# Optimization experiments

Hardware: AMD Instinct MI355X
Metric: run time of the kernel (lower is better)

Reference implementation:

```python
import jax, jax.numpy as jnp
import numpy as np

N, IN_DIM, HID, OUT = 100000, 256, 256, 128
E = 500000


def setup_inputs() -> dict:
    key = jax.random.key(0)
    ks = jax.random.split(key, 12)
    s_in = 1.0 / np.sqrt(IN_DIM)
    s_h = 1.0 / np.sqrt(HID)
    s_c = 1.0 / np.sqrt(2 * OUT)
    return {
        "x": jax.random.normal(ks[0], (N, IN_DIM), dtype=jnp.float32),
        "pos_u": jax.random.randint(ks[1], (E,), 0, N),
        "pos_v": jax.random.randint(ks[2], (E,), 0, N),
        "neg_u": jax.random.randint(ks[3], (E,), 0, N),
        "neg_v": jax.random.randint(ks[4], (E,), 0, N),
        "Wn1": jax.random.normal(ks[5], (IN_DIM, HID), dtype=jnp.float32) * s_in,
        "bn1": jnp.zeros((HID,), dtype=jnp.float32),
        "Wn2": jax.random.normal(ks[6], (HID, OUT), dtype=jnp.float32) * s_h,
        "bn2": jnp.zeros((OUT,), dtype=jnp.float32),
        "Ws1": jax.random.normal(ks[7], (2 * OUT, HID), dtype=jnp.float32) * s_c,
        "bs1": jnp.zeros((HID,), dtype=jnp.float32),
        "Ws2": jax.random.normal(ks[8], (HID, 1), dtype=jnp.float32) * s_h,
        "bs2": jnp.zeros((1,), dtype=jnp.float32),
    }


def _pair_logits(H, u, v, Ws1, bs1, Ws2, bs2):
    hu = H[u]  # [E, OUT] gather
    hv = H[v]
    feats = jnp.concatenate([jnp.abs(hu - hv), hu * hv], axis=-1)  # [E, 2*OUT]
    h = jax.nn.relu(feats @ Ws1 + bs1)
    return (h @ Ws2 + bs2)[..., 0]  # [E]


def reference(x, pos_u, pos_v, neg_u, neg_v,
              Wn1, bn1, Wn2, bn2, Ws1, bs1, Ws2, bs2):
    # node encoder MLP (dropout = identity in eval)
    H = jax.nn.relu(x @ Wn1 + bn1) @ Wn2 + bn2  # [N, OUT]
    pos_logit = _pair_logits(H, pos_u, pos_v, Ws1, bs1, Ws2, bs2)
    neg_logit = _pair_logits(H, neg_u, neg_v, Ws1, bs1, Ws2, bs2)
    return (pos_logit, neg_logit, H)
```

## Files before the change

### kernel.cpp

```cpp
#include <hip/hip_runtime.h>

typedef unsigned short u16;
typedef __bf16 bf16x8 __attribute__((ext_vector_type(8)));
typedef float f32x4 __attribute__((ext_vector_type(4)));
typedef unsigned int u32x4 __attribute__((ext_vector_type(4)));

#define MFMA16(a, b, c) __builtin_amdgcn_mfma_f32_16x16x32_bf16((a), (b), (c), 0, 0, 0)

#define NNODE 100000
#define EDGES 500000
#define NPAIR 1000000

__device__ __forceinline__ u16 bf16bits(float f) {
  __bf16 h = (__bf16)f;
  return __builtin_bit_cast(unsigned short, h);
}

__global__ void prep_weights(const float* __restrict__ Wn1,
                             const float* __restrict__ Wn2,
                             const float* __restrict__ Ws1,
                             u16* __restrict__ ws) {
  int gid = blockIdx.x * 256 + threadIdx.x;
  const float* src;
  int ldn;
  u16* dst;
  int e;
  if (gid < 65536) {
    src = Wn1; ldn = 256; dst = ws; e = gid;
  } else if (gid < 98304) {
    src = Wn2; ldn = 128; dst = ws + 65536; e = gid - 65536;
  } else {
    src = Ws1; ldn = 256; dst = ws + 98304; e = gid - 98304;
  }
  int j = e & 7;
  int lane = (e >> 3) & 63;
  int s = (e >> 9) & 7;
  int nt = e >> 12;
  int n = (nt << 4) | (lane & 15);
  int k = (s << 5) | (((lane >> 4) & 3) << 3) | j;
  dst[e] = bf16bits(src[k * ldn + n]);
}

__launch_bounds__(256, 2)
__global__ void node_kernel(const float* __restrict__ x,
                            const u16* __restrict__ WnT1,
                            const u16* __restrict__ WnT2,
                            const float* __restrict__ bn1,
                            const float* __restrict__ bn2,
                            float* __restrict__ Hout,
                            u16* __restrict__ Hb) {
  __shared__ __align__(16) u16 buf[32768];
  const int tid = threadIdx.x;
  const int w = tid >> 6, l = tid & 63;
  const int lg = l >> 4, ll = l & 15;
  const int rowbase = blockIdx.x * 128 + w * 32;

  bf16x8 af[2][8];
#pragma unroll
  for (int m = 0; m < 2; m++) {
    int r = rowbase + m * 16 + ll;
    if (r > NNODE - 1) r = NNODE - 1;
    const float* xp = x + (long)r * 256 + lg * 8;
#pragma unroll
    for (int c = 0; c < 8; c++) {
      f32x4 a0 = *(const f32x4*)(xp + c * 32);
      f32x4 a1 = *(const f32x4*)(xp + c * 32 + 4);
      bf16x8 d;
#pragma unroll
      for (int j = 0; j < 4; j++) {
        d[j] = (__bf16)a0[j];
        d[j + 4] = (__bf16)a1[j];
      }
      af[m][c] = d;
    }
  }

  f32x4 acc[2][16];
#pragma unroll
  for (int nh = 0; nh < 2; nh++) {
    if (nh) __syncthreads();
    {
      const u32x4* src = (const u32x4*)(WnT1 + nh * 32768);
      u32x4* dstv = (u32x4*)buf;
#pragma unroll
      for (int i = 0; i < 16; i++) dstv[tid + i * 256] = src[tid + i * 256];
    }
    __syncthreads();
#pragma unroll
    for (int nt = 0; nt < 8; nt++) {
      int n = nh * 128 + nt * 16 + ll;
      float bv = bn1[n];
      f32x4 a0 = {bv, bv, bv, bv}, a1 = a0;
      const u16* bp = buf + nt * 4096 + l * 8;
#pragma unroll
      for (int s = 0; s < 8; s++) {
        bf16x8 bw = *(const bf16x8*)(bp + s * 512);
        a0 = MFMA16(af[0][s], bw, a0);
        a1 = MFMA16(af[1][s], bw, a1);
      }
      acc[0][nh * 8 + nt] = a0;
      acc[1][nh * 8 + nt] = a1;
    }
  }
  __syncthreads();

  const int hbase = w * 8192;
#pragma unroll
  for (int m = 0; m < 2; m++) {
#pragma unroll
    for (int q = 0; q < 16; q++) {
      int s2 = q >> 1;
      int k3 = ((q & 1) << 1) | (ll >> 3);
      int j = ll & 7;
      f32x4 a = acc[m][q];
#pragma unroll
      for (int t = 0; t < 4; t++) {
        int lane2 = k3 * 16 + lg * 4 + t;
        buf[hbase + ((m * 8 + s2) * 64 + lane2) * 8 + j] = bf16bits(fmaxf(a[t], 0.f));
      }
    }
  }

#pragma unroll
  for (int m = 0; m < 2; m++) {
#pragma unroll
    for (int s = 0; s < 8; s++) {
      af[m][s] = *(const bf16x8*)(buf + hbase + ((m * 8 + s) * 64 + l) * 8);
    }
  }

#pragma unroll
  for (int nt = 0; nt < 8; nt++) {
    int n = nt * 16 + ll;
    float bv = bn2[n];
    f32x4 a0 = {bv, bv, bv, bv}, a1 = a0;
    const u16* bp = WnT2 + nt * 4096 + l * 8;
#pragma unroll
    for (int s = 0; s < 8; s++) {
      bf16x8 bw = *(const bf16x8*)(bp + s * 512);
      a0 = MFMA16(af[0][s], bw, a0);
      a1 = MFMA16(af[1][s], bw, a1);
    }
#pragma unroll
    for (int t = 0; t < 4; t++) {
      int r0 = rowbase + lg * 4 + t;
      if (r0 < NNODE) {
        Hout[(long)r0 * 128 + n] = a0[t];
        if (Hb) Hb[(long)r0 * 128 + n] = bf16bits(a0[t]);
      }
      int r1 = rowbase + 16 + lg * 4 + t;
      if (r1 < NNODE) {
        Hout[(long)r1 * 128 + n] = a1[t];
        if (Hb) Hb[(long)r1 * 128 + n] = bf16bits(a1[t]);
      }
    }
  }
}

template <bool BF16H>
__launch_bounds__(512, 1)
__global__ void pair_kernel7(const void* __restrict__ Hsrc,
                             const int* __restrict__ pos_u,
                             const int* __restrict__ pos_v,
                             const int* __restrict__ neg_u,
                             const int* __restrict__ neg_v,
                             const u16* __restrict__ WsT,
                             const float* __restrict__ bs1,
                             const float* __restrict__ Ws2,
                             const float* __restrict__ bs2,
                             float* __restrict__ out) {
  __shared__ __align__(16) u16 buf[65536];
  __shared__ float cvec[512];
  const int tid = threadIdx.x;
  {
    const u32x4* src = (const u32x4*)WsT;
    u32x4* dstv = (u32x4*)buf;
#pragma unroll
    for (int i = 0; i < 16; i++) dstv[tid + i * 512] = src[tid + i * 512];
    cvec[tid] = (tid < 256) ? bs1[tid] : Ws2[tid - 256];
  }
  __syncthreads();

  const int w = tid >> 6, l = tid & 63;
  const int lg = l >> 4, ll = l & 15;
  const float b2 = bs2[0];

  const int nwaves = gridDim.x * 8;
  for (int tile = blockIdx.x * 8 + w; tile < 31250; tile += nwaves) {
    const int base = tile * 32;

    bf16x8 af[2][8];
#pragma unroll
    for (int m = 0; m < 2; m++) {
      int p = base + m * 16 + ll;
      bool pos = p < EDGES;
      int idx = pos ? p : p - EDGES;
      const int* ul = pos ? pos_u : neg_u;
      const int* vl = pos ? pos_v : neg_v;
      int u = ul[idx];
      int v = vl[idx];
      if constexpr (BF16H) {
        const u16* hu = (const u16*)Hsrc + (long)u * 128 + lg * 8;
        const u16* hv = (const u16*)Hsrc + (long)v * 128 + lg * 8;
#pragma unroll
        for (int c = 0; c < 4; c++) {
          bf16x8 a = *(const bf16x8*)(hu + c * 32);
          bf16x8 b = *(const bf16x8*)(hv + c * 32);
          bf16x8 d = a - b;
          u32x4 du = __builtin_bit_cast(u32x4, d) & 0x7FFF7FFFu;
          af[m][c] = __builtin_bit_cast(bf16x8, du);
          af[m][c + 4] = a * b;
        }
      } else {
        const float* hu = (const float*)Hsrc + (long)u * 128 + lg * 8;
        const float* hv = (const float*)Hsrc + (long)v * 128 + lg * 8;
#pragma unroll
        for (int c = 0; c < 4; c++) {
          f32x4 a0 = *(const f32x4*)(hu + c * 32);
          f32x4 a1 = *(const f32x4*)(hu + c * 32 + 4);
          f32x4 b0 = *(const f32x4*)(hv + c * 32);
          f32x4 b1 = *(const f32x4*)(hv + c * 32 + 4);
          bf16x8 d, pr;
#pragma unroll
          for (int j = 0; j < 4; j++) {
            d[j] = (__bf16)__builtin_fabsf(a0[j] - b0[j]);
            d[j + 4] = (__bf16)__builtin_fabsf(a1[j] - b1[j]);
            pr[j] = (__bf16)(a0[j] * b0[j]);
            pr[j + 4] = (__bf16)(a1[j] * b1[j]);
          }
          af[m][c] = d;
          af[m][c + 4] = pr;
        }
      }
      __builtin_amdgcn_sched_barrier(0);
    }

    float lp[2][4] = {};
#pragma unroll
    for (int nt = 0; nt < 16; nt++) {
      float bv = cvec[nt * 16 + ll];
      f32x4 acc0 = {bv, bv, bv, bv}, acc1 = acc0;
      const u16* bp = buf + nt * 4096 + l * 8;
#pragma unroll
      for (int s = 0; s < 8; s++) {
        bf16x8 bw = *(const bf16x8*)(bp + s * 512);
        acc0 = MFMA16(af[0][s], bw, acc0);
        acc1 = MFMA16(af[1][s], bw, acc1);
      }
      float w2 = cvec[256 + nt * 16 + ll];
#pragma unroll
      for (int t = 0; t < 4; t++) {
        lp[0][t] += fmaxf(acc0[t], 0.f) * w2;
        lp[1][t] += fmaxf(acc1[t], 0.f) * w2;
      }
    }

#pragma unroll
    for (int m = 0; m < 2; m++) {
#pragma unroll
      for (int t = 0; t < 4; t++) {
        float v = lp[m][t];
        v += __shfl_xor(v, 1, 16);
        v += __shfl_xor(v, 2, 16);
        v += __shfl_xor(v, 4, 16);
        v += __shfl_xor(v, 8, 16);
        if (ll == 0) out[base + m * 16 + lg * 4 + t] = v + b2;
      }
    }
  }
}

extern "C" void kernel_launch(void* const* d_in, const int* in_sizes, int n_in,
                              void* d_out, int out_size, void* d_ws, size_t ws_size,
                              hipStream_t stream) {
  (void)in_sizes; (void)n_in; (void)out_size;
  const float* x = (const float*)d_in[0];
  const int* pos_u = (const int*)d_in[1];
  const int* pos_v = (const int*)d_in[2];
  const int* neg_u = (const int*)d_in[3];
  const int* neg_v = (const int*)d_in[4];
  const float* Wn1 = (const float*)d_in[5];
  const float* bn1 = (const float*)d_in[6];
  const float* Wn2 = (const float*)d_in[7];
  const float* bn2 = (const float*)d_in[8];
  const float* Ws1 = (const float*)d_in[9];
  const float* bs1 = (const float*)d_in[10];
  const float* Ws2 = (const float*)d_in[11];
  const float* bs2 = (const float*)d_in[12];
  float* out = (float*)d_out;
  u16* wsp = (u16*)d_ws;

  float* Hout = out + NPAIR;
  const size_t need = 327680 + (size_t)NNODE * 128 * 2;
  const bool bf16h = ws_size >= need;
  u16* Hb = bf16h ? (wsp + 163840) : nullptr;

  prep_weights<<<640, 256, 0, stream>>>(Wn1, Wn2, Ws1, wsp);
  node_kernel<<<(NNODE + 127) / 128, 256, 0, stream>>>(x, wsp, wsp + 65536, bn1, bn2,
                                                       Hout, Hb);
  if (bf16h) {
    pair_kernel7<true><<<256, 512, 0, stream>>>(Hb, pos_u, pos_v, neg_u, neg_v,
                                                wsp + 98304, bs1, Ws2, bs2, out);
  } else {
    pair_kernel7<false><<<256, 512, 0, stream>>>(Hout, pos_u, pos_v, neg_u, neg_v,
                                                 wsp + 98304, bs1, Ws2, bs2, out);
  }
}
```

Before: 255.3 us.

## Halve pair-kernel LDS by streaming Ws1 in two halves per chunk

The pair kernel now holds only half of the transposed Ws1 (64 KB instead of 128 KB) in shared memory. Each block processes a chunk of 256 pairs and reloads the other half between two barrier-separated passes, alternating which half stays resident. The smaller LDS footprint is meant to allow two blocks per CU, and the grid doubles to 512. In exchange, every chunk pays a 64 KB LDS reload from global/L2 plus two block-wide barriers. Bias and Ws2 values are read from global memory instead of a shared cache.

```diff
diff --git a/kernel.cpp b/kernel.cpp
--- a/kernel.cpp
+++ b/kernel.cpp
@@ -159,7 +159,7 @@
 
 template <bool BF16H>
 __launch_bounds__(512, 1)
-__global__ void pair_kernel7(const void* __restrict__ Hsrc,
+__global__ void pair_kernel9(const void* __restrict__ Hsrc,
                              const int* __restrict__ pos_u,
                              const int* __restrict__ pos_v,
                              const int* __restrict__ neg_u,
@@ -169,32 +169,32 @@
                              const float* __restrict__ Ws2,
                              const float* __restrict__ bs2,
                              float* __restrict__ out) {
-  __shared__ __align__(16) u16 buf[65536];
-  __shared__ float cvec[512];
+  __shared__ __align__(16) u16 buf[32768];
   const int tid = threadIdx.x;
+  const int w = tid >> 6, l = tid & 63;
+  const int lg = l >> 4, ll = l & 15;
+  const float b2 = bs2[0];
+
   {
     const u32x4* src = (const u32x4*)WsT;
     u32x4* dstv = (u32x4*)buf;
 #pragma unroll
-    for (int i = 0; i < 16; i++) dstv[tid + i * 512] = src[tid + i * 512];
-    cvec[tid] = (tid < 256) ? bs1[tid] : Ws2[tid - 256];
+    for (int i = 0; i < 8; i++) dstv[tid + i * 512] = src[tid + i * 512];
   }
   __syncthreads();
 
-  const int w = tid >> 6, l = tid & 63;
-  const int lg = l >> 4, ll = l & 15;
-  const float b2 = bs2[0];
-
-  const int nwaves = gridDim.x * 8;
-  for (int tile = blockIdx.x * 8 + w; tile < 31250; tile += nwaves) {
-    const int base = tile * 32;
+  int res = 0;
+  const int nchunks = (NPAIR + 255) / 256;
+  for (int chunk = blockIdx.x; chunk < nchunks; chunk += gridDim.x) {
+    const int base = chunk * 256 + w * 32;
 
     bf16x8 af[2][8];
 #pragma unroll
     for (int m = 0; m < 2; m++) {
       int p = base + m * 16 + ll;
-      bool pos = p < EDGES;
-      int idx = pos ? p : p - EDGES;
+      int pc = (p < NPAIR) ? p : (NPAIR - 1);
+      bool pos = pc < EDGES;
+      int idx = pos ? pc : pc - EDGES;
       const int* ul = pos ? pos_u : neg_u;
       const int* vl = pos ? pos_v : neg_v;
       int u = ul[idx];
@@ -236,9 +236,11 @@
     }
 
     float lp[2][4] = {};
-#pragma unroll
-    for (int nt = 0; nt < 16; nt++) {
-      float bv = cvec[nt * 16 + ll];
+
+#pragma unroll
+    for (int nt = 0; nt < 8; nt++) {
+      int n = res * 128 + nt * 16 + ll;
+      float bv = bs1[n];
       f32x4 acc0 = {bv, bv, bv, bv}, acc1 = acc0;
       const u16* bp = buf + nt * 4096 + l * 8;
 #pragma unroll
@@ -247,13 +249,43 @@
         acc0 = MFMA16(af[0][s], bw, acc0);
         acc1 = MFMA16(af[1][s], bw, acc1);
       }
-      float w2 = cvec[256 + nt * 16 + ll];
+      float w2 = Ws2[n];
 #pragma unroll
       for (int t = 0; t < 4; t++) {
         lp[0][t] += fmaxf(acc0[t], 0.f) * w2;
         lp[1][t] += fmaxf(acc1[t], 0.f) * w2;
       }
     }
+
+    __syncthreads();
+    {
+      const u32x4* src = (const u32x4*)(WsT + (res ^ 1) * 32768);
+      u32x4* dstv = (u32x4*)buf;
+#pragma unroll
+      for (int i = 0; i < 8; i++) dstv[tid + i * 512] = src[tid + i * 512];
+    }
+    __syncthreads();
+
+#pragma unroll
+    for (int nt = 0; nt < 8; nt++) {
+      int n = (res ^ 1) * 128 + nt * 16 + ll;
+      float bv = bs1[n];
+      f32x4 acc0 = {bv, bv, bv, bv}, acc1 = acc0;
+      const u16* bp = buf + nt * 4096 + l * 8;
+#pragma unroll
+      for (int s = 0; s < 8; s++) {
+        bf16x8 bw = *(const bf16x8*)(bp + s * 512);
+        acc0 = MFMA16(af[0][s], bw, acc0);
+        acc1 = MFMA16(af[1][s], bw, acc1);
+      }
+      float w2 = Ws2[n];
+#pragma unroll
+      for (int t = 0; t < 4; t++) {
+        lp[0][t] += fmaxf(acc0[t], 0.f) * w2;
+        lp[1][t] += fmaxf(acc1[t], 0.f) * w2;
+      }
+    }
+    res ^= 1;
 
 #pragma unroll
     for (int m = 0; m < 2; m++) {
@@ -264,7 +296,8 @@
         v += __shfl_xor(v, 2, 16);
         v += __shfl_xor(v, 4, 16);
         v += __shfl_xor(v, 8, 16);
-        if (ll == 0) out[base + m * 16 + lg * 4 + t] = v + b2;
+        int p = base + m * 16 + lg * 4 + t;
+        if (ll == 0 && p < NPAIR) out[p] = v + b2;
       }
     }
   }
@@ -299,10 +332,10 @@
   node_kernel<<<(NNODE + 127) / 128, 256, 0, stream>>>(x, wsp, wsp + 65536, bn1, bn2,
                                                        Hout, Hb);
   if (bf16h) {
-    pair_kernel7<true><<<256, 512, 0, stream>>>(Hb, pos_u, pos_v, neg_u, neg_v,
+    pair_kernel9<true><<<512, 512, 0, stream>>>(Hb, pos_u, pos_v, neg_u, neg_v,
                                                 wsp + 98304, bs1, Ws2, bs2, out);
   } else {
-    pair_kernel7<false><<<256, 512, 0, stream>>>(Hout, pos_u, pos_v, neg_u, neg_v,
+    pair_kernel9<false><<<512, 512, 0, stream>>>(Hout, pos_u, pos_v, neg_u, neg_v,
                                                  wsp + 98304, bs1, Ws2, bs2, out);
   }
 }
```

After: 279.7 us. 9.5% more time.
